# Kernel optimization log

Measured on AMD Instinct MI355X. Metric: run time of the kernel, lower is better.

The kernel has to match this reference:

```python
import jax, jax.numpy as jnp
import numpy as np

N, E, D, STEPS, MOLS, OUT = 50000, 400000, 128, 3, 256, 32


def setup_inputs() -> dict:
    key = jax.random.key(0)
    ks = jax.random.split(key, 20)
    s = 0.1  # weight scale ~ 1/sqrt(fan_in) to keep relu chain stable
    inp = {
        "states": jax.random.normal(ks[0], (N, D), jnp.float32),
        "Win": jax.random.normal(ks[1], (STEPS, 2 * D, 64), jnp.float32) * s,
        "b_in": jax.random.normal(ks[2], (STEPS, 64), jnp.float32) * s,
        "Wh": jax.random.normal(ks[3], (STEPS, 64, 64), jnp.float32) * s,
        "b_h": jax.random.normal(ks[4], (STEPS, 64), jnp.float32) * s,
        "Wout": jax.random.normal(ks[5], (STEPS, 64, D), jnp.float32) * s,
        "b_out": jax.random.normal(ks[6], (STEPS, D), jnp.float32) * s,
        "fc1_w": jax.random.normal(ks[7], (D, 64), jnp.float32) * s,
        "fc1_b": jax.random.normal(ks[8], (64,), jnp.float32) * s,
        "fc2_w": jax.random.normal(ks[9], (64, 64), jnp.float32) * s,
        "fc2_b": jax.random.normal(ks[10], (64,), jnp.float32) * s,
        "out_w": jax.random.normal(ks[11], (64, OUT), jnp.float32) * s,
        "out_b": jax.random.normal(ks[12], (OUT,), jnp.float32) * s,
        "src": jax.random.randint(ks[13], (E,), 0, N, jnp.int32).astype(jnp.int64),
        "dst": jax.random.randint(ks[14], (E,), 0, N, jnp.int32).astype(jnp.int64),
        "mol_ids": jax.random.randint(ks[15], (N,), 0, MOLS, jnp.int32).astype(jnp.int64),
        "num_mols": MOLS,
    }
    return inp


def reference(states, Win, b_in, Wh, b_h, Wout, b_out,
              fc1_w, fc1_b, fc2_w, fc2_b, out_w, out_b,
              src, dst, mol_ids, num_mols):
    n_atoms = states.shape[0]
    s = states
    for t in range(Win.shape[0]):  # message_steps (small, static)
        # per-edge message input: concat(owner state, neighbor state) -> [E, 2D]
        x = jnp.concatenate([s[dst], s[src]], axis=-1)
        m = jax.nn.relu(x @ Win[t] + b_in[t])
        m = jax.nn.relu(m @ Wh[t] + b_h[t])
        m = jax.nn.relu(m @ Wout[t] + b_out[t])  # [E, D]
        # atom-wise sum aggregation of incoming messages
        s = jax.ops.segment_sum(m, dst, num_segments=n_atoms)
    # molecule representation: sum of final atom states per molecule
    mol_repr = jax.ops.segment_sum(s, mol_ids, num_segments=num_mols)  # [M, D]
    h = jax.nn.relu(mol_repr @ fc1_w + fc1_b)
    h = jax.nn.relu(h @ fc2_w + fc2_b)
    return h @ out_w + out_b  # [M, OUT]
```

## Files before the change

kernel.cpp:

```cpp
#include <hip/hip_runtime.h>

typedef unsigned long long u64;
typedef unsigned short ushort_t;

#define NA 50000
#define NE 400000
#define DF 128
#define HID 64
#define NMOL 256
#define NOUT 32
#define NSTEP 3
#define NPB 782

#define RNG 8192
#define NRNG 7
#define NCH 64
#define CHUNK 6250
#define NCHM 16
#define CHM 3125
#define NWB 336
#define HISTB (NRNG*NCH + NCHM + NWB)
#define SCATB (NRNG*NCH + NCHM)
#define MBUF_ROWS 160000

#define NT (NE / 16)
#define EBLK 1024
#define EGW (EBLK * 4)

typedef __attribute__((ext_vector_type(8))) unsigned short ushort8;
typedef __attribute__((ext_vector_type(4))) float f32x4;
typedef __attribute__((ext_vector_type(8))) _Float16 half8;
typedef __attribute__((ext_vector_type(2))) _Float16 half2_t;
typedef __attribute__((ext_vector_type(2))) __fp16 fp16x2;

static __device__ __forceinline__ ushort_t f2h(float f) {
  union { _Float16 h; ushort_t u; } v; v.h = (_Float16)f; return v.u;
}
static __device__ __forceinline__ float hlo(unsigned d) {
  union { unsigned u; half2_t h; } v; v.u = d; return (float)v.h[0];
}
static __device__ __forceinline__ float hhi(unsigned d) {
  union { unsigned u; half2_t h; } v; v.u = d; return (float)v.h[1];
}
static __device__ __forceinline__ unsigned pkrtz(float a, float b) {
  union { fp16x2 h; unsigned u; } v;
  v.h = __builtin_amdgcn_cvt_pkrtz(a, b);
  return v.u;
}

__global__ __launch_bounds__(256) void hist_all(
    const int* __restrict__ dst, const int* __restrict__ mol_ids,
    const float* __restrict__ Win, const float* __restrict__ Wh,
    const float* __restrict__ Wout,
    ushort_t* __restrict__ WpB, ushort_t* __restrict__ WhB,
    ushort_t* __restrict__ WoB,
    ushort_t* __restrict__ H, unsigned* __restrict__ MH,
    int* __restrict__ mcnt) {
  __shared__ unsigned hist[RNG];
  const int b = blockIdx.x, t = threadIdx.x;
  if (b < NRNG * NCH) {
    const int r = b / NCH, c = b % NCH;
    const int lo = r * RNG;
    for (int i = t; i < RNG; i += 256) hist[i] = 0;
    __syncthreads();
    const int base = c * CHUNK;
    for (int k = t; k < CHUNK; k += 256) {
      int d = dst[base + k];
      unsigned rel = (unsigned)(d - lo);
      if (rel < RNG) atomicAdd(&hist[rel], 1u);
    }
    __syncthreads();
    ushort_t* Hp = H + (u64)b * RNG;
    for (int i = t; i < RNG; i += 256) Hp[i] = (ushort_t)hist[i];
    return;
  }
  int b2 = b - NRNG * NCH;
  if (b2 < NCHM) {
    if (t < 256) hist[t] = 0;
    __syncthreads();
    const int base = b2 * CHM;
    for (int k = t; k < CHM; k += 256) atomicAdd(&hist[mol_ids[base + k]], 1u);
    __syncthreads();
    if (t < 256) {
      MH[b2 * 256 + t] = hist[t];
      if (hist[t]) atomicAdd(&mcnt[t], (int)hist[t]);
    }
    return;
  }
  int g = (b2 - NCHM) * 256 + t;
  if (g < 3 * 16384) {
    int tt = g / 16384, r = g % 16384;
    int j = r & 7, lane = (r >> 3) & 63, f = r >> 9;
    int kc = f & 3, nt = f >> 2;
    int k = kc * 32 + (lane >> 4) * 8 + j;
    int n = nt * 16 + (lane & 15);
    float v = (n < 64) ? Win[tt * 16384 + k * 64 + n]
                       : Win[tt * 16384 + (128 + k) * 64 + (n - 64)];
    WpB[g] = f2h(v);
  }
  int g2 = g - 3 * 16384;
  if (g2 >= 0 && g2 < 3 * 4096) {
    int tt = g2 / 4096, r = g2 % 4096;
    int j = r & 7, lane = (r >> 3) & 63, f = r >> 9;
    int kc = f & 1, nt = f >> 1;
    int k = kc * 32 + (lane >> 4) * 8 + j;
    int n = nt * 16 + (lane & 15);
    WhB[g2] = f2h(Wh[tt * 4096 + k * 64 + n]);
  }
  int g3 = g2 - 3 * 4096;
  if (g3 >= 0 && g3 < 3 * 8192) {
    int tt = g3 / 8192, r = g3 % 8192;
    int j = r & 7, lane = (r >> 3) & 63, f = r >> 9;
    int kc = f & 1, nt = f >> 1;
    int k = kc * 32 + (lane >> 4) * 8 + j;
    int n = nt * 16 + (lane & 15);
    WoB[g3] = f2h(Wout[tt * 8192 + k * 128 + n]);
  }
}

__global__ void col_scan(const ushort_t* __restrict__ H,
                         ushort_t* __restrict__ Orel, int* __restrict__ counts) {
  int bidx = blockIdx.x * 256 + threadIdx.x;
  if (bidx >= NA) return;
  int r = bidx >> 13, i = bidx & (RNG - 1);
  const ushort_t* Hp = H + ((u64)r * NCH) * RNG + i;
  unsigned acc = 0;
  for (int c = 0; c < NCH; c++) {
    Orel[(u64)c * NA + bidx] = (ushort_t)acc;
    acc += Hp[(u64)c * RNG];
  }
  counts[bidx] = (int)acc;
}

__global__ void scan_phase1(const int* __restrict__ counts, int* __restrict__ tmp,
                            int* __restrict__ blk,
                            const int* __restrict__ mcnt, int* __restrict__ mrow) {
  __shared__ int sh[1024];
  int t = threadIdx.x;
  int i = blockIdx.x * 1024 + t;
  sh[t] = (i < NA) ? counts[i] : 0;
  __syncthreads();
  for (int off = 1; off < 1024; off <<= 1) {
    int x = (t >= off) ? sh[t - off] : 0;
    __syncthreads();
    sh[t] += x;
    __syncthreads();
  }
  if (i < NA) tmp[i] = sh[t];
  if (t == 1023) blk[blockIdx.x] = sh[1023];
  if (blockIdx.x == gridDim.x - 1) {
    __syncthreads();
    sh[t] = (t < NMOL) ? mcnt[t] : 0;
    __syncthreads();
    for (int off = 1; off < NMOL; off <<= 1) {
      int x = (t >= off && t < NMOL) ? sh[t - off] : 0;
      __syncthreads();
      if (t < NMOL) sh[t] += x;
      __syncthreads();
    }
    if (t < NMOL) mrow[t + 1] = sh[t];
    if (t == 0) mrow[0] = 0;
  }
}

__global__ void scan_phase3(const int* __restrict__ tmp, const int* __restrict__ blk,
                            int* __restrict__ row_ptr,
                            int* __restrict__ ntmp, int* __restrict__ nblk) {
  __shared__ int sh[1024];
  __shared__ int spre_sh;
  int t = threadIdx.x;
  int bid = blockIdx.x;
  if (t < 64) {
    int v = (t < bid) ? blk[t] : 0;
    for (int off = 32; off; off >>= 1) v += __shfl_down(v, off);
    if (t == 0) spre_sh = v;
  }
  __syncthreads();
  int spre = spre_sh;
  int i = bid * 1024 + t;
  int nwin = 0;
  if (i < NA) {
    int re = tmp[i] + spre;
    int rs = (t == 0) ? spre : (tmp[i - 1] + spre);
    row_ptr[i + 1] = re;
    if (re > rs) nwin = ((re - 1) >> 2) - (rs >> 2) + 1;
  }
  if (i == 0) row_ptr[0] = 0;
  sh[t] = nwin;
  __syncthreads();
  for (int off = 1; off < 1024; off <<= 1) {
    int x = (t >= off) ? sh[t - off] : 0;
    __syncthreads();
    sh[t] += x;
    __syncthreads();
  }
  if (i < NA) ntmp[i] = sh[t];
  if (t == 1023) nblk[bid] = sh[1023];
}

__global__ void nscan_p3(const int* __restrict__ ntmp, const int* __restrict__ nblk,
                         const int* __restrict__ row_ptr,
                         int* __restrict__ orow, int* __restrict__ orow2) {
  __shared__ int spre_sh;
  int t = threadIdx.x;
  int bid = blockIdx.x;
  if (t < 64) {
    int v = (t < bid) ? nblk[t] : 0;
    for (int off = 32; off; off >>= 1) v += __shfl_down(v, off);
    if (t == 0) spre_sh = v;
  }
  __syncthreads();
  int spre = spre_sh;
  int i = bid * 1024 + t;
  if (i < NA) {
    orow[i + 1] = ntmp[i] + spre;
    int oi = (t == 0) ? spre : (ntmp[i - 1] + spre);
    orow2[i] = oi - (row_ptr[i] >> 2);
  }
  if (i == 0) orow[0] = 0;
}

__global__ __launch_bounds__(256) void scat_all(
    const int* __restrict__ dst, const int* __restrict__ src,
    const int* __restrict__ row_ptr, const ushort_t* __restrict__ Orel,
    unsigned* __restrict__ ds_pack,
    const int* __restrict__ mol_ids, const int* __restrict__ mrow,
    const unsigned* __restrict__ MH, int* __restrict__ mol_sorted) {
  __shared__ unsigned cnt[RNG];
  __shared__ unsigned mbase[256];
  const int b = blockIdx.x, t = threadIdx.x;
  if (b < NRNG * NCH) {
    const int r = b / NCH, c = b % NCH;
    const int lo = r * RNG;
    for (int i = t; i < RNG; i += 256) cnt[i] = 0;
    __syncthreads();
    const int base = c * CHUNK;
    const ushort_t* Op = Orel + (u64)c * NA;
    for (int k = t; k < CHUNK; k += 256) {
      int e = base + k;
      int d = dst[e];
      unsigned rel = (unsigned)(d - lo);
      if (rel < RNG) {
        unsigned lr = atomicAdd(&cnt[rel], 1u);
        int pos = row_ptr[d] + (int)Op[d] + (int)lr;
        ds_pack[pos] = ((unsigned)d << 16) | (unsigned)src[e];
      }
    }
    return;
  }
  const int c2 = b - NRNG * NCH;
  if (t < 256) {
    unsigned s = (unsigned)mrow[t];
    for (int cp = 0; cp < c2; cp++) s += MH[cp * 256 + t];
    mbase[t] = s;
    cnt[t] = 0;
  }
  __syncthreads();
  const int base = c2 * CHM;
  for (int k = t; k < CHM; k += 256) {
    int a = base + k;
    int m = mol_ids[a];
    unsigned lr = atomicAdd(&cnt[m], 1u);
    mol_sorted[mbase[m] + lr] = a;
  }
}

__global__ __launch_bounds__(256) void node_proj(
    const float* __restrict__ s_in, const ushort_t* __restrict__ WpB,
    const float* __restrict__ b_in, ushort_t* __restrict__ PQb) {
  const int t = threadIdx.x;
  const int lane = t & 63, wv = t >> 6, quad = lane >> 4, l15 = lane & 15;
  const int n0 = blockIdx.x * 64 + wv * 16;
  int n = n0 + l15; if (n >= NA) n = NA - 1;
  union { half8 v; unsigned d[4]; } a[4];
#pragma unroll
  for (int c = 0; c < 4; c++) {
    const float* p = s_in + (u64)n * 128 + c * 32 + quad * 8;
    float4 f0 = *(const float4*)(p);
    float4 f1 = *(const float4*)(p + 4);
    a[c].d[0] = pkrtz(f0.x, f0.y);
    a[c].d[1] = pkrtz(f0.z, f0.w);
    a[c].d[2] = pkrtz(f1.x, f1.y);
    a[c].d[3] = pkrtz(f1.z, f1.w);
  }
  float binv[4];
#pragma unroll
  for (int nt = 0; nt < 4; nt++) binv[nt] = b_in[nt * 16 + l15];
#pragma unroll
  for (int nt = 0; nt < 8; nt++) {
    f32x4 acc = {0.f, 0.f, 0.f, 0.f};
#pragma unroll
    for (int c = 0; c < 4; c++) {
      half8 b = *(const half8*)&WpB[((nt * 4 + c) * 64 + lane) * 8];
      acc = __builtin_amdgcn_mfma_f32_16x16x32_f16(a[c].v, b, acc, 0, 0, 0);
    }
    float bias = (nt < 4) ? binv[nt] : 0.f;
#pragma unroll
    for (int r = 0; r < 4; r++) {
      int nn = n0 + quad * 4 + r;
      if (nn < NA) PQb[(u64)nn * 128 + nt * 16 + l15] = f2h(acc[r] + bias);
    }
  }
}

__global__ __launch_bounds__(256) void edge_msg(
    const ushort_t* __restrict__ PQb,
    const ushort_t* __restrict__ WhB, const ushort_t* __restrict__ WoB,
    const float* __restrict__ b_h, const float* __restrict__ b_out,
    const unsigned* __restrict__ ds_pack, const int* __restrict__ orow2,
    unsigned* __restrict__ m_buf) {
  __shared__ ushort_t h2s[4][16 * 72];
  const int t = threadIdx.x;
  const int lane = t & 63, wv = t >> 6, quad = lane >> 4, l15 = lane & 15;
  const int gw = blockIdx.x * 4 + wv;

  float bh[4], bo[8];
#pragma unroll
  for (int nt = 0; nt < 4; nt++) bh[nt] = b_h[nt * 16 + l15];
#pragma unroll
  for (int nt = 0; nt < 8; nt++) bo[nt] = b_out[nt * 16 + l15];

  ushort_t* hb = h2s[wv];
  const int colq = quad * 8;
  const half2_t z2 = {(_Float16)0.f, (_Float16)0.f};

  struct Ctx {
    int e;
    unsigned pk;
    int o;
    ushort8 pv0, pv1, qv0, qv1;
  };

  auto load_pk = [&](Ctx& c, int tile) {
    c.e = tile * 16 + l15;
    c.pk = ds_pack[c.e];
  };
  auto gather = [&](Ctx& c) {
    u64 da = c.pk >> 16, sa = c.pk & 0xffffu;
    c.o = orow2[da] + (c.e >> 2);
    c.pv0 = *(const ushort8*)&PQb[da * 128 + colq];
    c.pv1 = *(const ushort8*)&PQb[da * 128 + 32 + colq];
    c.qv0 = *(const ushort8*)&PQb[sa * 128 + 64 + colq];
    c.qv1 = *(const ushort8*)&PQb[sa * 128 + 96 + colq];
  };
  auto compute = [&](Ctx& c) {
    union UPQ { ushort8 u; half2_t h[4]; };
    UPQ P0, P1, Q0, Q1;
    P0.u = c.pv0; P1.u = c.pv1; Q0.u = c.qv0; Q1.u = c.qv1;
    union { half8 v; half2_t h[4]; } a1[2];
#pragma unroll
    for (int k = 0; k < 4; k++) {
      half2_t s0 = P0.h[k] + Q0.h[k];
      half2_t s1 = P1.h[k] + Q1.h[k];
      a1[0].h[k] = __builtin_elementwise_max(s0, z2);
      a1[1].h[k] = __builtin_elementwise_max(s1, z2);
    }
#pragma unroll
    for (int nt = 0; nt < 4; nt++) {
      f32x4 acc = {0.f, 0.f, 0.f, 0.f};
#pragma unroll
      for (int cc = 0; cc < 2; cc++) {
        half8 b = *(const half8*)&WhB[((nt * 2 + cc) * 64 + lane) * 8];
        acc = __builtin_amdgcn_mfma_f32_16x16x32_f16(a1[cc].v, b, acc, 0, 0, 0);
      }
#pragma unroll
      for (int r = 0; r < 4; r++)
        hb[(quad * 4 + r) * 72 + nt * 16 + l15] =
            f2h(fmaxf(acc[r] + bh[nt], 0.f));
    }
    half8 a2[2];
    a2[0] = *(const half8*)&hb[l15 * 72 + colq];
    a2[1] = *(const half8*)&hb[l15 * 72 + 32 + colq];
    f32x4 acc2[8];
#pragma unroll
    for (int nt = 0; nt < 8; nt++) {
      f32x4 acc = {0.f, 0.f, 0.f, 0.f};
#pragma unroll
      for (int cc = 0; cc < 2; cc++) {
        half8 b = *(const half8*)&WoB[((nt * 2 + cc) * 64 + lane) * 8];
        acc = __builtin_amdgcn_mfma_f32_16x16x32_f16(a2[cc], b, acc, 0, 0, 0);
      }
      acc2[nt] = acc;
    }
    int pkr[4], orr[4];
#pragma unroll
    for (int r = 0; r < 4; r++) {
      int srcl = (lane & 48) + quad * 4 + r;
      pkr[r] = __shfl((int)c.pk, srcl);
      orr[r] = __shfl(c.o, srcl);
    }
    unsigned prev = ((unsigned)pkr[0]) >> 16;
    int orow_ = orr[0];
    float run[8];
#pragma unroll
    for (int nt = 0; nt < 8; nt++) run[nt] = 0.f;
#pragma unroll
    for (int r = 0; r < 4; r++) {
      unsigned dcur = ((unsigned)pkr[r]) >> 16;
      if (dcur != prev) {
        unsigned* rowp = m_buf + (u64)orow_ * 64;
#pragma unroll
        for (int k = 0; k < 4; k++)
          rowp[k * 16 + l15] = pkrtz(run[2 * k], run[2 * k + 1]);
#pragma unroll
        for (int nt = 0; nt < 8; nt++) run[nt] = 0.f;
        prev = dcur; orow_ = orr[r];
      }
#pragma unroll
      for (int nt = 0; nt < 8; nt++)
        run[nt] += fmaxf(acc2[nt][r] + bo[nt], 0.f);
    }
    unsigned* rowp = m_buf + (u64)orow_ * 64;
#pragma unroll
    for (int k = 0; k < 4; k++)
      rowp[k * 16 + l15] = pkrtz(run[2 * k], run[2 * k + 1]);
  };

  Ctx A, B, C;
  int tc = gw;
  load_pk(A, tc);
  int tb = tc + EGW;
  if (tb < NT) load_pk(B, tb);
  gather(A);
  while (tc < NT) {
    int tn = tc + EGW;
    if (tn < NT) gather(B);
    int t2 = tn + EGW;
    if (t2 < NT) load_pk(C, t2);
    compute(A);
    A = B; B = C;
    tc = tn;
  }
}

__global__ __launch_bounds__(256) void agg_proj(
    const unsigned* __restrict__ m_buf, const int* __restrict__ orow,
    const ushort_t* __restrict__ WpB, const float* __restrict__ b_in,
    ushort_t* __restrict__ PQb) {
  __shared__ ushort_t a_s[64 * 136];
  __shared__ int obs_s[65];
  const int t = threadIdx.x;
  const int lane = t & 63, wv = t >> 6, quad = lane >> 4, l15 = lane & 15;
  const int n0 = blockIdx.x * 64;
  if (t < 65) {
    int idx = n0 + t; if (idx > NA) idx = NA;
    obs_s[t] = orow[idx];
  }
  __syncthreads();

  for (int r = 0; r < 16; r++) {
    const int d = n0 + wv * 16 + r;
    float s0 = 0.f, s1 = 0.f;
    if (d < NA) {
      int ob = obs_s[wv * 16 + r], oe = obs_s[wv * 16 + r + 1];
      int n = oe - ob;
      float t0 = 0.f, t1 = 0.f, u0 = 0.f, u1 = 0.f, v0 = 0.f, v1 = 0.f;
      int full = n & ~3;
      int e = ob;
      for (; e < ob + full; e += 4) {
        unsigned w0 = m_buf[(u64)(e + 0) * 64 + lane];
        unsigned w1 = m_buf[(u64)(e + 1) * 64 + lane];
        unsigned w2 = m_buf[(u64)(e + 2) * 64 + lane];
        unsigned w3 = m_buf[(u64)(e + 3) * 64 + lane];
        s0 += hlo(w0); s1 += hhi(w0);
        t0 += hlo(w1); t1 += hhi(w1);
        u0 += hlo(w2); u1 += hhi(w2);
        v0 += hlo(w3); v1 += hhi(w3);
      }
      int rem = n - full;
      if (rem > 0) {
        int i1 = (rem > 1) ? e + 1 : e;
        int i2 = (rem > 2) ? e + 2 : e;
        unsigned w0 = m_buf[(u64)e * 64 + lane];
        unsigned w1 = m_buf[(u64)i1 * 64 + lane];
        unsigned w2 = m_buf[(u64)i2 * 64 + lane];
        s0 += hlo(w0); s1 += hhi(w0);
        if (rem > 1) { t0 += hlo(w1); t1 += hhi(w1); }
        if (rem > 2) { u0 += hlo(w2); u1 += hhi(w2); }
      }
      s0 = (s0 + t0) + (u0 + v0);
      s1 = (s1 + t1) + (u1 + v1);
    }
    const int row = wv * 16 + r;
    a_s[row * 136 + quad * 32 + l15] = f2h(s0);
    a_s[row * 136 + quad * 32 + 16 + l15] = f2h(s1);
  }

  float binv[4];
#pragma unroll
  for (int nt = 0; nt < 4; nt++) binv[nt] = b_in[nt * 16 + l15];
  half8 a[4];
#pragma unroll
  for (int c = 0; c < 4; c++)
    a[c] = *(const half8*)&a_s[(wv * 16 + l15) * 136 + c * 32 + quad * 8];
#pragma unroll
  for (int nt = 0; nt < 8; nt++) {
    f32x4 acc = {0.f, 0.f, 0.f, 0.f};
#pragma unroll
    for (int c = 0; c < 4; c++) {
      half8 b = *(const half8*)&WpB[((nt * 4 + c) * 64 + lane) * 8];
      acc = __builtin_amdgcn_mfma_f32_16x16x32_f16(a[c], b, acc, 0, 0, 0);
    }
    float bias = (nt < 4) ? binv[nt] : 0.f;
#pragma unroll
    for (int r = 0; r < 4; r++) {
      int nn = n0 + wv * 16 + quad * 4 + r;
      if (nn < NA) PQb[(u64)nn * 128 + nt * 16 + l15] = f2h(acc[r] + bias);
    }
  }
}

__global__ __launch_bounds__(256) void agg_mol2(
    const unsigned* __restrict__ m_buf, const int* __restrict__ orow,
    const int* __restrict__ mol_sorted, const int* __restrict__ mol_ids,
    float* __restrict__ mol_repr) {
  __shared__ int mids[64], obs[64], oes[64];
  const int t = threadIdx.x;
  const int lane = t & 63, wv = t >> 6;
  const int base = blockIdx.x * 64;
  if (t < 64) {
    int idx = base + t;
    int r = (idx < NA) ? mol_sorted[idx] : 0;
    mids[t] = (idx < NA) ? mol_ids[r] : -1;
    obs[t] = orow[r];
    oes[t] = orow[r + 1];
  }
  __syncthreads();
  const int c0 = (lane >> 4) * 32 + (lane & 15);
  float r0 = 0.f, r1 = 0.f;
  int prev = mids[wv * 16];
  for (int i = 0; i < 16; i++) {
    int li = wv * 16 + i;
    int m = mids[li];
    if (m != prev) {
      if (prev >= 0) {
        atomicAdd(&mol_repr[(u64)prev * 128 + c0], r0);
        atomicAdd(&mol_repr[(u64)prev * 128 + c0 + 16], r1);
      }
      r0 = 0.f; r1 = 0.f; prev = m;
    }
    if (m >= 0) {
      int ob = obs[li], oe = oes[li];
      int n = oe - ob;
      float t0 = 0.f, t1 = 0.f, u0 = 0.f, u1 = 0.f, v0 = 0.f, v1 = 0.f;
      int full = n & ~3;
      int e = ob;
      for (; e < ob + full; e += 4) {
        unsigned w0 = m_buf[(u64)(e + 0) * 64 + lane];
        unsigned w1 = m_buf[(u64)(e + 1) * 64 + lane];
        unsigned w2 = m_buf[(u64)(e + 2) * 64 + lane];
        unsigned w3 = m_buf[(u64)(e + 3) * 64 + lane];
        r0 += hlo(w0); r1 += hhi(w0);
        t0 += hlo(w1); t1 += hhi(w1);
        u0 += hlo(w2); u1 += hhi(w2);
        v0 += hlo(w3); v1 += hhi(w3);
      }
      int rem = n - full;
      if (rem > 0) {
        int i1 = (rem > 1) ? e + 1 : e;
        int i2 = (rem > 2) ? e + 2 : e;
        unsigned w0 = m_buf[(u64)e * 64 + lane];
        unsigned w1 = m_buf[(u64)i1 * 64 + lane];
        unsigned w2 = m_buf[(u64)i2 * 64 + lane];
        r0 += hlo(w0); r1 += hhi(w0);
        if (rem > 1) { t0 += hlo(w1); t1 += hhi(w1); }
        if (rem > 2) { u0 += hlo(w2); u1 += hhi(w2); }
      }
      r0 += (t0 + u0) + v0;
      r1 += (t1 + u1) + v1;
    }
  }
  if (prev >= 0) {
    atomicAdd(&mol_repr[(u64)prev * 128 + c0], r0);
    atomicAdd(&mol_repr[(u64)prev * 128 + c0 + 16], r1);
  }
}

__global__ void final_mlp(const float* __restrict__ mol_repr,
                          const float* __restrict__ fc1_w, const float* __restrict__ fc1_b,
                          const float* __restrict__ fc2_w, const float* __restrict__ fc2_b,
                          const float* __restrict__ out_w, const float* __restrict__ out_b,
                          float* __restrict__ out) {
  int m = blockIdx.x, j = threadIdx.x;
  __shared__ float h1sh[64], h2sh[64];
  const float* mr = mol_repr + (u64)m * DF;
  float acc = fc1_b[j];
  for (int d = 0; d < DF; d++) acc = fmaf(mr[d], fc1_w[d * 64 + j], acc);
  h1sh[j] = fmaxf(acc, 0.f);
  __syncthreads();
  acc = fc2_b[j];
  for (int k = 0; k < 64; k++) acc = fmaf(h1sh[k], fc2_w[k * 64 + j], acc);
  h2sh[j] = fmaxf(acc, 0.f);
  __syncthreads();
  if (j < NOUT) {
    acc = out_b[j];
    for (int k = 0; k < 64; k++) acc = fmaf(h2sh[k], out_w[k * NOUT + j], acc);
    out[(u64)m * NOUT + j] = acc;
  }
}

extern "C" void kernel_launch(void* const* d_in, const int* in_sizes, int n_in,
                              void* d_out, int out_size, void* d_ws, size_t ws_size,
                              hipStream_t stream) {
  const float* states = (const float*)d_in[0];
  const float* Win    = (const float*)d_in[1];
  const float* b_in   = (const float*)d_in[2];
  const float* Wh     = (const float*)d_in[3];
  const float* b_h    = (const float*)d_in[4];
  const float* Wout   = (const float*)d_in[5];
  const float* b_out  = (const float*)d_in[6];
  const float* fc1_w  = (const float*)d_in[7];
  const float* fc1_b  = (const float*)d_in[8];
  const float* fc2_w  = (const float*)d_in[9];
  const float* fc2_b  = (const float*)d_in[10];
  const float* out_w  = (const float*)d_in[11];
  const float* out_b  = (const float*)d_in[12];
  const int* src      = (const int*)d_in[13];
  const int* dst      = (const int*)d_in[14];
  const int* mol_ids  = (const int*)d_in[15];

  char* ws = (char*)d_ws;
  u64 o = 0;
  auto alloc = [&](u64 bytes) {
    void* p = ws + o;
    o += (bytes + 255) & ~255ull;
    return p;
  };
  unsigned* m_buf = (unsigned*)alloc((u64)MBUF_ROWS * 64 * 4);
  ushort_t* PQb  = (ushort_t*)alloc((u64)NA * DF * 2);
  ushort_t* WpB  = (ushort_t*)alloc(3 * 16384 * 2);
  ushort_t* WhB  = (ushort_t*)alloc(3 * 4096 * 2);
  ushort_t* WoB  = (ushort_t*)alloc(3 * 8192 * 2);
  char* zbase    = ws + o;
  float* molr    = (float*)alloc((u64)NMOL * DF * 4);
  int* mcnt      = (int*)alloc(NMOL * 4);
  u64 zbytes     = (u64)((ws + o) - zbase);
  int* counts    = (int*)alloc((u64)NA * 4);
  int* row_ptr   = (int*)alloc((u64)(NA + 1) * 4);
  int* mrow      = (int*)alloc((NMOL + 1) * 4);
  unsigned* ds_pack = (unsigned*)alloc((u64)NE * 4);
  int* mol_sorted = (int*)alloc((u64)NA * 4);
  int* scan_tmp  = (int*)alloc((u64)NA * 4);
  int* blk_sums  = (int*)alloc(64 * 4);
  int* ntmp      = (int*)alloc((u64)NA * 4);
  int* nblk      = (int*)alloc(64 * 4);
  int* orow      = (int*)alloc((u64)(NA + 1) * 4);
  int* orow2     = (int*)alloc((u64)NA * 4);
  ushort_t* H    = (ushort_t*)alloc((u64)NRNG * NCH * RNG * 2);
  ushort_t* Orel = (ushort_t*)alloc((u64)NCH * NA * 2);
  unsigned* MH   = (unsigned*)alloc((u64)NCHM * 256 * 4);
  (void)ws_size; (void)in_sizes; (void)n_in; (void)out_size;

  const int NSCAN = (NA + 1023) / 1024;

  hipMemsetAsync(zbase, 0, zbytes, stream);

  hist_all<<<HISTB, 256, 0, stream>>>(dst, mol_ids, Win, Wh, Wout,
                                      WpB, WhB, WoB, H, MH, mcnt);
  col_scan<<<(NA + 255) / 256, 256, 0, stream>>>(H, Orel, counts);
  scan_phase1<<<NSCAN, 1024, 0, stream>>>(counts, scan_tmp, blk_sums, mcnt, mrow);
  scan_phase3<<<NSCAN, 1024, 0, stream>>>(scan_tmp, blk_sums, row_ptr, ntmp, nblk);
  nscan_p3<<<NSCAN, 1024, 0, stream>>>(ntmp, nblk, row_ptr, orow, orow2);
  scat_all<<<SCATB, 256, 0, stream>>>(dst, src, row_ptr, Orel, ds_pack,
                                      mol_ids, mrow, MH, mol_sorted);

  node_proj<<<NPB, 256, 0, stream>>>(states, WpB, b_in, PQb);
  for (int t = 0; t < NSTEP; t++) {
    edge_msg<<<EBLK, 256, 0, stream>>>(
        PQb, WhB + t * 4096, WoB + t * 8192,
        b_h + t * 64, b_out + t * 128, ds_pack, orow2, m_buf);
    if (t < NSTEP - 1) {
      agg_proj<<<(NA + 63) / 64, 256, 0, stream>>>(m_buf, orow,
                                                   WpB + (t + 1) * 16384,
                                                   b_in + (t + 1) * 64, PQb);
    } else {
      agg_mol2<<<(NA + 63) / 64, 256, 0, stream>>>(m_buf, orow, mol_sorted,
                                                   mol_ids, molr);
    }
  }
  final_mlp<<<NMOL, 64, 0, stream>>>(molr, fc1_w, fc1_b, fc2_w, fc2_b, out_w, out_b,
                                     (float*)d_out);
}
```

Measured before the change: 284.0 us.

## Merge per-edge partial sums over 8-edge windows via cross-quad shuffle

```diff
diff --git a/kernel.cpp b/kernel.cpp
--- a/kernel.cpp
+++ b/kernel.cpp
@@ -14,14 +14,14 @@
 
 #define RNG 8192
 #define NRNG 7
-#define NCH 64
-#define CHUNK 6250
+#define NCH 32
+#define CHUNK 12500
 #define NCHM 16
 #define CHM 3125
 #define NWB 336
 #define HISTB (NRNG*NCH + NCHM + NWB)
 #define SCATB (NRNG*NCH + NCHM)
-#define MBUF_ROWS 160000
+#define MBUF_ROWS 110000
 
 #define NT (NE / 16)
 #define EBLK 1024
@@ -183,7 +183,7 @@
     int re = tmp[i] + spre;
     int rs = (t == 0) ? spre : (tmp[i - 1] + spre);
     row_ptr[i + 1] = re;
-    if (re > rs) nwin = ((re - 1) >> 2) - (rs >> 2) + 1;
+    if (re > rs) nwin = ((re - 1) >> 3) - (rs >> 3) + 1;
   }
   if (i == 0) row_ptr[0] = 0;
   sh[t] = nwin;
@@ -215,7 +215,7 @@
   if (i < NA) {
     orow[i + 1] = ntmp[i] + spre;
     int oi = (t == 0) ? spre : (ntmp[i - 1] + spre);
-    orow2[i] = oi - (row_ptr[i] >> 2);
+    orow2[i] = oi - (row_ptr[i] >> 3);
   }
   if (i == 0) orow[0] = 0;
 }
@@ -337,7 +337,7 @@
   };
   auto gather = [&](Ctx& c) {
     u64 da = c.pk >> 16, sa = c.pk & 0xffffu;
-    c.o = orow2[da] + (c.e >> 2);
+    c.o = orow2[da] + (c.e >> 3);
     c.pv0 = *(const ushort8*)&PQb[da * 128 + colq];
     c.pv1 = *(const ushort8*)&PQb[da * 128 + 32 + colq];
     c.qv0 = *(const ushort8*)&PQb[sa * 128 + 64 + colq];
@@ -382,38 +382,84 @@
       }
       acc2[nt] = acc;
     }
-    int pkr[4], orr[4];
+    const int grp = lane & 48;
+    const int wb = (quad & 2) * 4;
+    const bool odd = (quad & 1) != 0;
+    const int jb = odd ? 4 : 0;
+    int pkd[8];
+#pragma unroll
+    for (int r = 0; r < 8; r++) pkd[r] = __shfl((int)c.pk, grp + wb + r);
+    int orr[4];
+#pragma unroll
+    for (int r = 0; r < 4; r++) orr[r] = __shfl(c.o, grp + quad * 4 + r);
+    const bool conn =
+        ((((unsigned)pkd[3]) >> 16) == (((unsigned)pkd[4]) >> 16));
+    unsigned dpre = ((unsigned)pkd[jb]) >> 16;
+    int cur_row = orr[0];
+    float run[8];
+    unsigned sx[4];
+    bool head_done = false;
+#pragma unroll
+    for (int nt = 0; nt < 8; nt++) run[nt] = 0.f;
+#pragma unroll
+    for (int k = 0; k < 4; k++) sx[k] = 0u;
 #pragma unroll
     for (int r = 0; r < 4; r++) {
-      int srcl = (lane & 48) + quad * 4 + r;
-      pkr[r] = __shfl((int)c.pk, srcl);
-      orr[r] = __shfl(c.o, srcl);
-    }
-    unsigned prev = ((unsigned)pkr[0]) >> 16;
-    int orow_ = orr[0];
-    float run[8];
-#pragma unroll
-    for (int nt = 0; nt < 8; nt++) run[nt] = 0.f;
-#pragma unroll
-    for (int r = 0; r < 4; r++) {
-      unsigned dcur = ((unsigned)pkr[r]) >> 16;
-      if (dcur != prev) {
-        unsigned* rowp = m_buf + (u64)orow_ * 64;
+      unsigned dcur = ((unsigned)pkd[jb + r]) >> 16;
+      if (dcur != dpre) {
+        unsigned w[4];
+#pragma unroll
+        for (int k = 0; k < 4; k++) w[k] = pkrtz(run[2 * k], run[2 * k + 1]);
+        if (!head_done) {
+          head_done = true;
+#pragma unroll
+          for (int k = 0; k < 4; k++) sx[k] = w[k];
+          if (!(odd && conn)) {
+            unsigned* rowp = m_buf + (u64)cur_row * 64;
+#pragma unroll
+            for (int k = 0; k < 4; k++) rowp[k * 16 + l15] = w[k];
+          }
+        } else {
+          unsigned* rowp = m_buf + (u64)cur_row * 64;
+#pragma unroll
+          for (int k = 0; k < 4; k++) rowp[k * 16 + l15] = w[k];
+        }
+#pragma unroll
+        for (int nt = 0; nt < 8; nt++) run[nt] = 0.f;
+        dpre = dcur; cur_row = orr[r];
+      }
+#pragma unroll
+      for (int nt = 0; nt < 8; nt++)
+        run[nt] += fmaxf(acc2[nt][r] + bo[nt], 0.f);
+    }
+    if (!head_done) {
+#pragma unroll
+      for (int k = 0; k < 4; k++) sx[k] = pkrtz(run[2 * k], run[2 * k + 1]);
+    }
+    unsigned rx[4];
+#pragma unroll
+    for (int k = 0; k < 4; k++)
+      rx[k] = (unsigned)__shfl_xor((int)sx[k], 16);
+    if (!odd) {
+      if (conn) {
+#pragma unroll
+        for (int k = 0; k < 4; k++) {
+          run[2 * k] += hlo(rx[k]);
+          run[2 * k + 1] += hhi(rx[k]);
+        }
+      }
+      unsigned* rowp = m_buf + (u64)cur_row * 64;
+#pragma unroll
+      for (int k = 0; k < 4; k++)
+        rowp[k * 16 + l15] = pkrtz(run[2 * k], run[2 * k + 1]);
+    } else {
+      if (!(conn && !head_done)) {
+        unsigned* rowp = m_buf + (u64)cur_row * 64;
 #pragma unroll
         for (int k = 0; k < 4; k++)
           rowp[k * 16 + l15] = pkrtz(run[2 * k], run[2 * k + 1]);
-#pragma unroll
-        for (int nt = 0; nt < 8; nt++) run[nt] = 0.f;
-        prev = dcur; orow_ = orr[r];
-      }
-#pragma unroll
-      for (int nt = 0; nt < 8; nt++)
-        run[nt] += fmaxf(acc2[nt][r] + bo[nt], 0.f);
-    }
-    unsigned* rowp = m_buf + (u64)orow_ * 64;
-#pragma unroll
-    for (int k = 0; k < 4; k++)
-      rowp[k * 16 + l15] = pkrtz(run[2 * k], run[2 * k + 1]);
+      }
+    }
   };
 
   Ctx A, B, C;
```

Result: slower. 375.4 us (+32.2%).

## Fuse column scan and three prefix-scan kernels into one decoupled-lookback kernel

Applied to the files above, without the earlier changes.

```diff
diff --git a/kernel.cpp b/kernel.cpp
--- a/kernel.cpp
+++ b/kernel.cpp
@@ -26,6 +26,8 @@
 #define NT (NE / 16)
 #define EBLK 1024
 #define EGW (EBLK * 4)
+
+#define NSCAN 49
 
 typedef __attribute__((ext_vector_type(8))) unsigned short ushort8;
 typedef __attribute__((ext_vector_type(4))) float f32x4;
@@ -118,27 +120,29 @@
   }
 }
 
-__global__ void col_scan(const ushort_t* __restrict__ H,
-                         ushort_t* __restrict__ Orel, int* __restrict__ counts) {
-  int bidx = blockIdx.x * 256 + threadIdx.x;
-  if (bidx >= NA) return;
-  int r = bidx >> 13, i = bidx & (RNG - 1);
-  const ushort_t* Hp = H + ((u64)r * NCH) * RNG + i;
-  unsigned acc = 0;
-  for (int c = 0; c < NCH; c++) {
-    Orel[(u64)c * NA + bidx] = (ushort_t)acc;
-    acc += Hp[(u64)c * RNG];
-  }
-  counts[bidx] = (int)acc;
-}
-
-__global__ void scan_phase1(const int* __restrict__ counts, int* __restrict__ tmp,
-                            int* __restrict__ blk,
-                            const int* __restrict__ mcnt, int* __restrict__ mrow) {
+__global__ __launch_bounds__(1024) void mega_scan(
+    const ushort_t* __restrict__ H, ushort_t* __restrict__ Orel,
+    int* __restrict__ row_ptr, int* __restrict__ orow, int* __restrict__ orow2,
+    const int* __restrict__ mcnt, int* __restrict__ mrow,
+    int* __restrict__ stA, int* __restrict__ stB) {
   __shared__ int sh[1024];
-  int t = threadIdx.x;
-  int i = blockIdx.x * 1024 + t;
-  sh[t] = (i < NA) ? counts[i] : 0;
+  __shared__ int pre_sh;
+  const int t = threadIdx.x, bid = blockIdx.x;
+  const int i = bid * 1024 + t;
+
+  int cnt = 0;
+  if (i < NA) {
+    int r = i >> 13, ii = i & (RNG - 1);
+    const ushort_t* Hp = H + ((u64)r * NCH) * RNG + ii;
+    unsigned acc = 0;
+    for (int c = 0; c < NCH; c++) {
+      Orel[(u64)c * NA + i] = (ushort_t)acc;
+      acc += Hp[(u64)c * RNG];
+    }
+    cnt = (int)acc;
+  }
+
+  sh[t] = cnt;
   __syncthreads();
   for (int off = 1; off < 1024; off <<= 1) {
     int x = (t >= off) ? sh[t - off] : 0;
@@ -146,9 +150,58 @@
     sh[t] += x;
     __syncthreads();
   }
-  if (i < NA) tmp[i] = sh[t];
-  if (t == 1023) blk[blockIdx.x] = sh[1023];
-  if (blockIdx.x == gridDim.x - 1) {
+  const int incl = sh[t];
+  if (t == 0) atomicExch(&stA[bid], sh[1023] + 1);
+  if (t < 64) {
+    int v = 0;
+    if (t < bid) {
+      do { v = atomicAdd(&stA[t], 0); } while (v == 0);
+      v -= 1;
+    }
+    for (int off = 32; off; off >>= 1) v += __shfl_down(v, off);
+    if (t == 0) pre_sh = v;
+  }
+  __syncthreads();
+  const int excl1 = pre_sh;
+
+  int rs = 0, nwin = 0;
+  if (i < NA) {
+    int re = excl1 + incl;
+    rs = re - cnt;
+    row_ptr[i + 1] = re;
+    if (re > rs) nwin = ((re - 1) >> 2) - (rs >> 2) + 1;
+  }
+  if (i == 0) row_ptr[0] = 0;
+  __syncthreads();
+
+  sh[t] = nwin;
+  __syncthreads();
+  for (int off = 1; off < 1024; off <<= 1) {
+    int x = (t >= off) ? sh[t - off] : 0;
+    __syncthreads();
+    sh[t] += x;
+    __syncthreads();
+  }
+  const int incl2 = sh[t];
+  if (t == 0) atomicExch(&stB[bid], sh[1023] + 1);
+  if (t < 64) {
+    int v = 0;
+    if (t < bid) {
+      do { v = atomicAdd(&stB[t], 0); } while (v == 0);
+      v -= 1;
+    }
+    for (int off = 32; off; off >>= 1) v += __shfl_down(v, off);
+    if (t == 0) pre_sh = v;
+  }
+  __syncthreads();
+  const int excl2 = pre_sh;
+  if (i < NA) {
+    orow[i + 1] = excl2 + incl2;
+    orow2[i] = (excl2 + incl2 - nwin) - (rs >> 2);
+  }
+  if (i == 0) orow[0] = 0;
+
+  if (bid == NSCAN - 1) {
     __syncthreads();
     sh[t] = (t < NMOL) ? mcnt[t] : 0;
     __syncthreads();
@@ -161,63 +214,6 @@
     if (t < NMOL) mrow[t + 1] = sh[t];
     if (t == 0) mrow[0] = 0;
   }
-}
-
-__global__ void scan_phase3(const int* __restrict__ tmp, const int* __restrict__ blk,
-                            int* __restrict__ row_ptr,
-                            int* __restrict__ ntmp, int* __restrict__ nblk) {
-  __shared__ int sh[1024];
-  __shared__ int spre_sh;
-  int t = threadIdx.x;
-  int bid = blockIdx.x;
-  if (t < 64) {
-    int v = (t < bid) ? blk[t] : 0;
-    for (int off = 32; off; off >>= 1) v += __shfl_down(v, off);
-    if (t == 0) spre_sh = v;
-  }
-  __syncthreads();
-  int spre = spre_sh;
-  int i = bid * 1024 + t;
-  int nwin = 0;
-  if (i < NA) {
-    int re = tmp[i] + spre;
-    int rs = (t == 0) ? spre : (tmp[i - 1] + spre);
-    row_ptr[i + 1] = re;
-    if (re > rs) nwin = ((re - 1) >> 2) - (rs >> 2) + 1;
-  }
-  if (i == 0) row_ptr[0] = 0;
-  sh[t] = nwin;
-  __syncthreads();
-  for (int off = 1; off < 1024; off <<= 1) {
-    int x = (t >= off) ? sh[t - off] : 0;
-    __syncthreads();
-    sh[t] += x;
-    __syncthreads();
-  }
-  if (i < NA) ntmp[i] = sh[t];
-  if (t == 1023) nblk[bid] = sh[1023];
-}
-
-__global__ void nscan_p3(const int* __restrict__ ntmp, const int* __restrict__ nblk,
-                         const int* __restrict__ row_ptr,
-                         int* __restrict__ orow, int* __restrict__ orow2) {
-  __shared__ int spre_sh;
-  int t = threadIdx.x;
-  int bid = blockIdx.x;
-  if (t < 64) {
-    int v = (t < bid) ? nblk[t] : 0;
-    for (int off = 32; off; off >>= 1) v += __shfl_down(v, off);
-    if (t == 0) spre_sh = v;
-  }
-  __syncthreads();
-  int spre = spre_sh;
-  int i = bid * 1024 + t;
-  if (i < NA) {
-    orow[i + 1] = ntmp[i] + spre;
-    int oi = (t == 0) ? spre : (ntmp[i - 1] + spre);
-    orow2[i] = oi - (row_ptr[i] >> 2);
-  }
-  if (i == 0) orow[0] = 0;
 }
 
 __global__ __launch_bounds__(256) void scat_all(
@@ -634,16 +630,13 @@
   char* zbase    = ws + o;
   float* molr    = (float*)alloc((u64)NMOL * DF * 4);
   int* mcnt      = (int*)alloc(NMOL * 4);
+  int* stA       = (int*)alloc(64 * 4);
+  int* stB       = (int*)alloc(64 * 4);
   u64 zbytes     = (u64)((ws + o) - zbase);
-  int* counts    = (int*)alloc((u64)NA * 4);
   int* row_ptr   = (int*)alloc((u64)(NA + 1) * 4);
   int* mrow      = (int*)alloc((NMOL + 1) * 4);
   unsigned* ds_pack = (unsigned*)alloc((u64)NE * 4);
   int* mol_sorted = (int*)alloc((u64)NA * 4);
-  int* scan_tmp  = (int*)alloc((u64)NA * 4);
-  int* blk_sums  = (int*)alloc(64 * 4);
-  int* ntmp      = (int*)alloc((u64)NA * 4);
-  int* nblk      = (int*)alloc(64 * 4);
   int* orow      = (int*)alloc((u64)(NA + 1) * 4);
   int* orow2     = (int*)alloc((u64)NA * 4);
   ushort_t* H    = (ushort_t*)alloc((u64)NRNG * NCH * RNG * 2);
@@ -651,16 +644,12 @@
   unsigned* MH   = (unsigned*)alloc((u64)NCHM * 256 * 4);
   (void)ws_size; (void)in_sizes; (void)n_in; (void)out_size;
 
-  const int NSCAN = (NA + 1023) / 1024;
-
   hipMemsetAsync(zbase, 0, zbytes, stream);
 
   hist_all<<<HISTB, 256, 0, stream>>>(dst, mol_ids, Win, Wh, Wout,
                                       WpB, WhB, WoB, H, MH, mcnt);
-  col_scan<<<(NA + 255) / 256, 256, 0, stream>>>(H, Orel, counts);
-  scan_phase1<<<NSCAN, 1024, 0, stream>>>(counts, scan_tmp, blk_sums, mcnt, mrow);
-  scan_phase3<<<NSCAN, 1024, 0, stream>>>(scan_tmp, blk_sums, row_ptr, ntmp, nblk);
-  nscan_p3<<<NSCAN, 1024, 0, stream>>>(ntmp, nblk, row_ptr, orow, orow2);
+  mega_scan<<<NSCAN, 1024, 0, stream>>>(H, Orel, row_ptr, orow, orow2,
+                                        mcnt, mrow, stA, stB);
   scat_all<<<SCATB, 256, 0, stream>>>(dst, src, row_ptr, Orel, ds_pack,
                                       mol_ids, mrow, MH, mol_sorted);
 
```

After: 283.1 us. No clear change (-0.3%).
